# Performance work log

Measured on AMD Instinct MI355X. Metric: run time of the kernel, lower is better.

## Reference

```python
import jax, jax.numpy as jnp
import numpy as np

# Model dims
H = 1024          # hidden_size
I = 2048          # intermediate_size
E = 8             # num_experts
IE = I // E       # expert_intermediate_size = 256
V = 100000        # vocab_size
B, S = 8, 2048


def _rowwise_quantize(x):
    """Dynamic per-row int8 quantization (faithful to dynamic_quantize_int8, per_channel=True).
    Returns quantized values kept in float32 (identical values to int8->float cast) and per-row scale."""
    max_vals = jnp.max(jnp.abs(x), axis=-1, keepdims=True)
    scale = jnp.maximum(max_vals / 127.0, 1e-8)
    x_q = jnp.clip(jnp.round(x / scale), -128.0, 127.0)
    return x_q, scale[..., 0]


def _quantize_weight(w):
    """Per-output-channel int8 quantization of a [K, N] weight (as in from_float)."""
    max_vals = jnp.max(jnp.abs(w), axis=0, keepdims=True)      # [1, N]
    scale = jnp.maximum(max_vals / 127.0, 1e-8)
    w_q = jnp.clip(jnp.round(w / scale), -128.0, 127.0).astype(jnp.int8)
    return w_q, scale[0]


def setup_inputs() -> dict:
    key = jax.random.key(0)
    ks = jax.random.split(key, 6)
    hidden_states = jax.random.normal(ks[0], (B, S, H), dtype=jnp.float32)
    token_ids = jax.random.randint(ks[1], (B, S), 0, V, dtype=jnp.int32)

    # Pre-quantized expert weights (int8) with per-output-channel fp32 scales.
    gate_w = jax.random.normal(ks[2], (E, H, IE), dtype=jnp.float32) * 0.02
    up_w = jax.random.normal(ks[3], (E, H, IE), dtype=jnp.float32) * 0.02
    down_w = jax.random.normal(ks[4], (E, IE, H), dtype=jnp.float32) * 0.02
    gate_q, gate_scale = jax.vmap(_quantize_weight)(gate_w)   # [E,H,IE] int8, [E,IE]
    up_q, up_scale = jax.vmap(_quantize_weight)(up_w)         # [E,H,IE] int8, [E,IE]
    down_q, down_scale = jax.vmap(_quantize_weight)(down_w)   # [E,IE,H] int8, [E,H]

    # Deterministic contiguous token->expert mapping (V divisible by E here).
    token_to_expert = jnp.minimum(jnp.arange(V, dtype=jnp.int32) // (V // E), E - 1)

    return {
        "hidden_states": hidden_states,
        "token_ids": token_ids,
        "gate_q": gate_q, "gate_scale": gate_scale,
        "up_q": up_q, "up_scale": up_scale,
        "down_q": down_q, "down_scale": down_scale,
        "token_to_expert": token_to_expert,
    }


def reference(hidden_states, token_ids, gate_q, gate_scale, up_q, up_scale,
              down_q, down_scale, token_to_expert):
    Bh, Sh, Hh = hidden_states.shape
    n_exp = gate_q.shape[0]
    vocab = token_to_expert.shape[0]

    tid = jnp.clip(token_ids, 0, vocab - 1)
    expert_ids = token_to_expert[tid].reshape(-1)             # [T]

    x = hidden_states.reshape(-1, Hh)                          # [T, H]
    # Per-row activation quantization is expert-independent -> do it once for all tokens.
    x_q, x_s = _rowwise_quantize(x)                            # [T,H], [T]

    gq = gate_q.astype(jnp.float32)
    uq = up_q.astype(jnp.float32)
    dq = down_q.astype(jnp.float32)

    out = jnp.zeros_like(x)
    for e in range(n_exp):  # small fixed expert count
        # fused quantize-GEMM: int8 matmul + per-row activation scale + per-col weight scale
        gate = (x_q @ gq[e]) * x_s[:, None] * gate_scale[e][None, :]   # [T, IE]
        up = (x_q @ uq[e]) * x_s[:, None] * up_scale[e][None, :]       # [T, IE]
        inter = jax.nn.silu(gate) * up
        i_q, i_s = _rowwise_quantize(inter)
        o = (i_q @ dq[e]) * i_s[:, None] * down_scale[e][None, :]      # [T, H]
        out = jnp.where((expert_ids == e)[:, None], o, out)
    return out.reshape(Bh, Sh, Hh)
```

## Files before the change

kernel.cpp:

```cpp
#include <hip/hip_runtime.h>

typedef int   int4v   __attribute__((ext_vector_type(4)));
typedef float float4v __attribute__((ext_vector_type(4)));

#define T_TOK 16384
#define HD    1024
#define IE    256
#define EN    8
#define VSZ   100000

#define M_OFF 16
#define M_TS1 25

#define XQ_OFF   0ull
#define PB1_OFF  21053440ull
#define PB2_OFF  25247744ull
#define PERM_OFF 27344896ull
#define XS_OFF   27410688ull
#define META_OFF 27542272ull
#define BC_OFF   27542528ull
#define BB_OFF   27544576ull

__device__ __forceinline__ void gload16(const void* g, void* l) {
    __builtin_amdgcn_global_load_lds(
        (const __attribute__((address_space(1))) unsigned int*)g,
        (__attribute__((address_space(3))) unsigned int*)l,
        16, 0, 0);
}

__global__ void k_hist(const int* __restrict__ ids, const int* __restrict__ t2e,
                       int* __restrict__ bc) {
    __shared__ int h[EN];
    if (threadIdx.x < EN) h[threadIdx.x] = 0;
    __syncthreads();
    int t = blockIdx.x * 256 + threadIdx.x;
    int id = ids[t]; id = min(max(id, 0), VSZ - 1);
    atomicAdd(&h[t2e[id]], 1);
    __syncthreads();
    if (threadIdx.x < EN) bc[blockIdx.x * EN + threadIdx.x] = h[threadIdx.x];
}

__global__ __launch_bounds__(512) void k_scan(const int* __restrict__ bc,
                                              int* __restrict__ bbase,
                                              int* __restrict__ meta) {
    int e = threadIdx.x >> 6;
    int b = threadIdx.x & 63;
    int c = bc[b * EN + e];
    int inc = c;
    #pragma unroll
    for (int s = 1; s < 64; s <<= 1) {
        int v = __shfl_up(inc, s, 64);
        if (b >= s) inc += v;
    }
    int exc = inc - c;
    __shared__ int tot[EN];
    __shared__ int goff[EN];
    if (b == 63) tot[e] = inc;
    __syncthreads();
    if (threadIdx.x == 0) {
        int off = 0, t1 = 0;
        meta[M_OFF] = 0; meta[M_TS1] = 0;
        #pragma unroll
        for (int i = 0; i < EN; ++i) {
            goff[i] = off;
            int cc = tot[i];
            off += cc; t1 += (cc + 31) >> 5;
            meta[M_OFF + i + 1] = off;
            meta[M_TS1 + i + 1] = t1;
        }
    }
    __syncthreads();
    bbase[b * EN + e] = goff[e] + exc;
}

__global__ void k_assign(const int* __restrict__ ids, const int* __restrict__ t2e,
                         const int* __restrict__ bbase, int* __restrict__ perm) {
    __shared__ int cur[EN];
    if (threadIdx.x < EN) cur[threadIdx.x] = bbase[blockIdx.x * EN + threadIdx.x];
    __syncthreads();
    int t = blockIdx.x * 256 + threadIdx.x;
    int id = ids[t]; id = min(max(id, 0), VSZ - 1);
    int e = t2e[id];
    int slot = atomicAdd(&cur[e], 1);
    perm[slot] = t;
}

__global__ __launch_bounds__(256) void k_pre(const float* __restrict__ hidden,
                                             const int* __restrict__ gq,
                                             const int* __restrict__ uq,
                                             const int* __restrict__ dq,
                                             signed char* __restrict__ xq,
                                             float* __restrict__ xs,
                                             signed char* __restrict__ pb1,
                                             signed char* __restrict__ pb2) {
    int b = blockIdx.x;
    if (b < 4096) {
        int w = threadIdx.x >> 6, lane = threadIdx.x & 63;
        int token = (b << 2) + w;
        const float* row = hidden + (size_t)token * HD;
        float v[16];
        #pragma unroll
        for (int j = 0; j < 4; ++j) {
            float4v f = *(const float4v*)(row + lane * 16 + j * 4);
            v[j*4+0] = f[0]; v[j*4+1] = f[1]; v[j*4+2] = f[2]; v[j*4+3] = f[3];
        }
        float mx = 0.0f;
        #pragma unroll
        for (int j = 0; j < 16; ++j) mx = fmaxf(mx, fabsf(v[j]));
        #pragma unroll
        for (int s = 1; s < 64; s <<= 1) mx = fmaxf(mx, __shfl_xor(mx, s, 64));
        float sc = fmaxf(mx / 127.0f, 1e-8f);
        if (lane == 0) xs[token] = sc;
        int4v pk;
        #pragma unroll
        for (int j = 0; j < 4; ++j) {
            int bb[4];
            #pragma unroll
            for (int u = 0; u < 4; ++u) {
                float t = rintf(v[j*4+u] / sc);
                t = fminf(fmaxf(t, -128.0f), 127.0f);
                bb[u] = (int)t;
            }
            pk[j] = (bb[0] & 255) | ((bb[1] & 255) << 8) | ((bb[2] & 255) << 16) | (bb[3] << 24);
        }
        *(int4v*)(xq + (size_t)token * HD + lane * 16) = pk;
    } else {
        int idx = (b - 4096) * 256 + threadIdx.x;
        if (idx < 262144) {
            int n = idx & 511, kc = (idx >> 9) & 63, e = idx >> 15;
            const int* src = (n < 256) ? gq + (((size_t)((e << 10) + (kc << 4)) << 8) + n)
                                       : uq + (((size_t)((e << 10) + (kc << 4)) << 8) + (n - 256));
            int4v pk;
            #pragma unroll
            for (int jj = 0; jj < 4; ++jj) {
                int b0 = src[(size_t)(jj * 4 + 0) << 8], b1 = src[(size_t)(jj * 4 + 1) << 8];
                int b2 = src[(size_t)(jj * 4 + 2) << 8], b3 = src[(size_t)(jj * 4 + 3) << 8];
                pk[jj] = (b0 & 255) | ((b1 & 255) << 8) | ((b2 & 255) << 16) | (b3 << 24);
            }
            *(int4v*)(pb1 + ((size_t)((((e << 6) + kc) << 9) + n) << 4)) = pk;
        } else {
            int j = idx - 262144;
            int n = j & 1023, kc = (j >> 10) & 15, e = j >> 14;
            const int* src = dq + (((size_t)((e << 8) + (kc << 4)) << 10) + n);
            int4v pk;
            #pragma unroll
            for (int jj = 0; jj < 4; ++jj) {
                int b0 = src[(size_t)(jj * 4 + 0) << 10], b1 = src[(size_t)(jj * 4 + 1) << 10];
                int b2 = src[(size_t)(jj * 4 + 2) << 10], b3 = src[(size_t)(jj * 4 + 3) << 10];
                pk[jj] = (b0 & 255) | ((b1 & 255) << 8) | ((b2 & 255) << 16) | (b3 << 24);
            }
            *(int4v*)(pb2 + ((size_t)((((e << 4) + kc) << 10) + n) << 4)) = pk;
        }
    }
}

__global__ __launch_bounds__(256, 2) void k_mlp(const signed char* __restrict__ xq,
                                                const signed char* __restrict__ pb1,
                                                const signed char* __restrict__ pb2,
                                                const float* __restrict__ xs,
                                                const float* __restrict__ gsc,
                                                const float* __restrict__ usc,
                                                const float* __restrict__ dsc,
                                                const int* __restrict__ meta,
                                                const int* __restrict__ perm,
                                                float* __restrict__ out) {
    int b = (blockIdx.x & 7) * 65 + (blockIdx.x >> 3);
    int e = -1, m0 = 0, gend = 0;
    #pragma unroll
    for (int i = 0; i < EN; ++i) {
        int s0 = meta[M_TS1 + i], s1 = meta[M_TS1 + i + 1];
        if (b >= s0 && b < s1) { e = i; m0 = meta[M_OFF + i] + ((b - s0) << 5); gend = meta[M_OFF + i + 1]; }
    }
    if (e < 0) return;
    const int w = threadIdx.x >> 6, lane = threadIdx.x & 63;
    const int q = lane >> 4, r = lane & 15;

    __shared__ __align__(16) signed char lB[2][32768];
    __shared__ __align__(16) signed char arena[8192];
    float* pmax = (float*)(arena + 4096);
    float* rsc  = (float*)(arena + 4608);
    int*   ptok = (int*)(arena + 4736);

    if (threadIdx.x < 32) ptok[threadIdx.x] = perm[min(m0 + (int)threadIdx.x, T_TOK - 1)];
    __syncthreads();

    int tokr[2][4];
    #pragma unroll
    for (int mi = 0; mi < 2; ++mi)
        #pragma unroll
        for (int g = 0; g < 4; ++g)
            tokr[mi][g] = ptok[(mi << 4) + (q << 2) + g];

    const signed char* pbe1 = pb1 + (size_t)e * (64 * 512 * 16);
    const signed char* pbe2 = pb2 + (size_t)e * (16 * 1024 * 16);
    const int arow = (w << 4) + (lane >> 2);
    const int acq  = (lane & 3) ^ ((lane >> 2) & 3);
    const signed char* ga_base = xq + (size_t)ptok[arow & 31] * HD + (acq << 4);

    #define G1_STAGE(buf, kt)                                                          \
        {                                                                              \
            int kc0 = (kt) << 2;                                                       \
            _Pragma("unroll")                                                          \
            for (int j = 0; j < 8; ++j) {                                              \
                int n = ((j << 6) + lane) ^ ((w & 1) << 3);                            \
                gload16(pbe1 + (((size_t)(kc0 + w) * 512 + n) << 4),                   \
                        &lB[buf][((w << 3) + j) << 10]);                               \
            }                                                                          \
            if (w < 2) gload16(ga_base + ((kt) << 6), arena + ((buf) << 11) + (w << 10)); \
        }

    #define G2_STAGE(buf, st)                                                          \
        {                                                                              \
            int kc0 = ((st) & 3) << 2; int nhs = (st) >> 2;                            \
            _Pragma("unroll")                                                          \
            for (int j = 0; j < 8; ++j) {                                              \
                int n = ((j << 6) + lane) ^ ((w & 1) << 3);                            \
                gload16(pbe2 + (((size_t)(kc0 + w) * 1024 + (nhs << 9) + n) << 4),     \
                        &lB[buf][((w << 3) + j) << 10]);                               \
            }                                                                          \
        }

    int4v zero = {0, 0, 0, 0};
    int4v accg[2][4], accu[2][4];
    #pragma unroll
    for (int mi = 0; mi < 2; ++mi)
        #pragma unroll
        for (int i = 0; i < 4; ++i) { accg[mi][i] = zero; accu[mi][i] = zero; }

    G1_STAGE(0, 0);
    for (int kt = 0; kt < 16; ++kt) {
        int cur = kt & 1;
        __syncthreads();
        if (kt < 15) G1_STAGE(cur ^ 1, kt + 1);
        int4v a[2];
        #pragma unroll
        for (int mi = 0; mi < 2; ++mi)
            a[mi] = *(const int4v*)&arena[(cur << 11) + ((((mi << 4) + r) << 6) + ((q ^ (r & 3)) << 4))];
        #pragma unroll
        for (int i = 0; i < 4; ++i) {
            int n = (w << 6) + (i << 4) + r;
            int sg = (q << 9) + (n ^ ((q & 1) << 3));
            int su = (q << 9) + ((n + 256) ^ ((q & 1) << 3));
            int4v bg = *(const int4v*)&lB[cur][sg << 4];
            int4v bu = *(const int4v*)&lB[cur][su << 4];
            #pragma unroll
            for (int mi = 0; mi < 2; ++mi) {
                accg[mi][i] = __builtin_amdgcn_mfma_i32_16x16x64_i8(a[mi], bg, accg[mi][i], 0, 0, 0);
                accu[mi][i] = __builtin_amdgcn_mfma_i32_16x16x64_i8(a[mi], bu, accu[mi][i], 0, 0, 0);
            }
        }
    }
    #undef G1_STAGE

    G2_STAGE(0, 0);

    float gs[4], us[4];
    #pragma unroll
    for (int i = 0; i < 4; ++i) {
        int n = (w << 6) + (i << 4) + r;
        gs[i] = gsc[e * IE + n];
        us[i] = usc[e * IE + n];
    }
    float xsr[2][4];
    #pragma unroll
    for (int mi = 0; mi < 2; ++mi)
        #pragma unroll
        for (int g = 0; g < 4; ++g)
            xsr[mi][g] = xs[tokr[mi][g]];

    float inter[2][4][4];
    float pm[2][4];
    #pragma unroll
    for (int mi = 0; mi < 2; ++mi)
        #pragma unroll
        for (int g = 0; g < 4; ++g) {
            float mx = 0.0f;
            #pragma unroll
            for (int i = 0; i < 4; ++i) {
                float gv = (float)accg[mi][i][g] * xsr[mi][g] * gs[i];
                float uv = (float)accu[mi][i][g] * xsr[mi][g] * us[i];
                float sg = gv / (1.0f + expf(-gv));
                float vv = sg * uv;
                inter[mi][i][g] = vv;
                mx = fmaxf(mx, fabsf(vv));
            }
            #pragma unroll
            for (int s = 1; s < 16; s <<= 1) mx = fmaxf(mx, __shfl_xor(mx, s, 64));
            pm[mi][g] = mx;
        }

    __syncthreads();
    if (r == 0) {
        #pragma unroll
        for (int mi = 0; mi < 2; ++mi)
            #pragma unroll
            for (int g = 0; g < 4; ++g)
                pmax[(w << 5) + (mi << 4) + (q << 2) + g] = pm[mi][g];
    }
    __syncthreads();
    if (threadIdx.x < 32) {
        int row = threadIdx.x;
        float mx = fmaxf(fmaxf(pmax[row], pmax[32 + row]), fmaxf(pmax[64 + row], pmax[96 + row]));
        rsc[row] = fmaxf(mx / 127.0f, 1e-8f);
    }
    __syncthreads();
    float rscr[2][4];
    #pragma unroll
    for (int mi = 0; mi < 2; ++mi)
        #pragma unroll
        for (int g = 0; g < 4; ++g)
            rscr[mi][g] = rsc[(mi << 4) + (q << 2) + g];
    __syncthreads();

    #pragma unroll
    for (int mi = 0; mi < 2; ++mi)
        #pragma unroll
        for (int g = 0; g < 4; ++g) {
            int row = (mi << 4) + (q << 2) + g;
            float sc = rscr[mi][g];
            #pragma unroll
            for (int i = 0; i < 4; ++i) {
                float t = rintf(inter[mi][i][g] / sc);
                t = fminf(fmaxf(t, -128.0f), 127.0f);
                arena[(row << 8) + ((((w << 2) + i) ^ (row & 3)) << 4) + r] = (signed char)(int)t;
            }
        }

    int4v acc2[2][8];
    for (int st = 0; st < 8; ++st) {
        int cur = st & 1;
        __syncthreads();
        if (st < 7) G2_STAGE(cur ^ 1, st + 1);
        if ((st & 3) == 0) {
            #pragma unroll
            for (int mi = 0; mi < 2; ++mi)
                #pragma unroll
                for (int i = 0; i < 8; ++i) acc2[mi][i] = zero;
        }
        int4v a2[2];
        #pragma unroll
        for (int mi = 0; mi < 2; ++mi) {
            int row2 = (mi << 4) + r;
            a2[mi] = *(const int4v*)&arena[(row2 << 8) + (((((st & 3) << 2) + q) ^ (r & 3)) << 4)];
        }
        #pragma unroll
        for (int i = 0; i < 8; ++i) {
            int n = (w << 7) + (i << 4) + r;
            int sb = (q << 9) + (n ^ ((q & 1) << 3));
            int4v bb = *(const int4v*)&lB[cur][sb << 4];
            #pragma unroll
            for (int mi = 0; mi < 2; ++mi)
                acc2[mi][i] = __builtin_amdgcn_mfma_i32_16x16x64_i8(a2[mi], bb, acc2[mi][i], 0, 0, 0);
        }
        if ((st & 3) == 3) {
            int nhs = st >> 2;
            float ds[8];
            #pragma unroll
            for (int i = 0; i < 8; ++i)
                ds[i] = dsc[e * HD + (nhs << 9) + (w << 7) + (i << 4) + r];
            #pragma unroll
            for (int mi = 0; mi < 2; ++mi)
                #pragma unroll
                for (int g = 0; g < 4; ++g) {
                    int slot = m0 + (mi << 4) + (q << 2) + g;
                    if (slot < gend) {
                        size_t ob = (size_t)tokr[mi][g] * HD + (nhs << 9) + (w << 7) + r;
                        #pragma unroll
                        for (int i = 0; i < 8; ++i)
                            out[ob + (i << 4)] = (float)acc2[mi][i][g] * rscr[mi][g] * ds[i];
                    }
                }
        }
    }
    #undef G2_STAGE
}

extern "C" void kernel_launch(void* const* d_in, const int* in_sizes, int n_in,
                              void* d_out, int out_size, void* d_ws, size_t ws_size,
                              hipStream_t stream) {
    const float* hidden = (const float*)d_in[0];
    const int*   ids    = (const int*)d_in[1];
    const int*   gq     = (const int*)d_in[2];
    const float* gsc    = (const float*)d_in[3];
    const int*   uq     = (const int*)d_in[4];
    const float* usc    = (const float*)d_in[5];
    const int*   dq     = (const int*)d_in[6];
    const float* dsc    = (const float*)d_in[7];
    const int*   t2e    = (const int*)d_in[8];
    float* out = (float*)d_out;

    char* ws = (char*)d_ws;
    signed char* xq  = (signed char*)(ws + XQ_OFF);
    signed char* pb1 = (signed char*)(ws + PB1_OFF);
    signed char* pb2 = (signed char*)(ws + PB2_OFF);
    int*   perm = (int*)(ws + PERM_OFF);
    float* xs   = (float*)(ws + XS_OFF);
    int*   meta = (int*)(ws + META_OFF);
    int*   bc   = (int*)(ws + BC_OFF);
    int*   bbase= (int*)(ws + BB_OFF);

    k_hist<<<64, 256, 0, stream>>>(ids, t2e, bc);
    k_scan<<<1, 512, 0, stream>>>(bc, bbase, meta);
    k_assign<<<64, 256, 0, stream>>>(ids, t2e, bbase, perm);
    k_pre<<<5632, 256, 0, stream>>>(hidden, gq, uq, dq, xq, xs, pb1, pb2);
    k_mlp<<<520, 256, 0, stream>>>(xq, pb1, pb2, xs, gsc, usc, dsc, meta, perm, out);
}
```

Before: 204.6 us.

## Halve LDS staging buffers and load activations to registers for four-block occupancy

The per-stage weight buffers shrink from 32KB to 16KB each, and the gate and up tiles are now staged in alternate half-steps, doubling the pipeline step count. Activations are loaded straight from global memory into registers instead of through LDS, which also removes the token-index shared table and one barrier. Launch bounds rise from 2 to 4 blocks per CU to raise occupancy and hide latency. The cost is twice as many barriers per K loop and tighter register pressure, plus full unrolling of the loops.

```diff
diff --git a/kernel.cpp b/kernel.cpp
--- a/kernel.cpp
+++ b/kernel.cpp
@@ -154,7 +154,7 @@
     }
 }
 
-__global__ __launch_bounds__(256, 2) void k_mlp(const signed char* __restrict__ xq,
+__global__ __launch_bounds__(256, 4) void k_mlp(const signed char* __restrict__ xq,
                                                 const signed char* __restrict__ pb1,
                                                 const signed char* __restrict__ pb2,
                                                 const float* __restrict__ xs,
@@ -175,49 +175,44 @@
     const int w = threadIdx.x >> 6, lane = threadIdx.x & 63;
     const int q = lane >> 4, r = lane & 15;
 
-    __shared__ __align__(16) signed char lB[2][32768];
-    __shared__ __align__(16) signed char arena[8192];
-    float* pmax = (float*)(arena + 4096);
-    float* rsc  = (float*)(arena + 4608);
-    int*   ptok = (int*)(arena + 4736);
-
-    if (threadIdx.x < 32) ptok[threadIdx.x] = perm[min(m0 + (int)threadIdx.x, T_TOK - 1)];
-    __syncthreads();
-
-    int tokr[2][4];
-    #pragma unroll
-    for (int mi = 0; mi < 2; ++mi)
-        #pragma unroll
-        for (int g = 0; g < 4; ++g)
-            tokr[mi][g] = ptok[(mi << 4) + (q << 2) + g];
+    __shared__ __align__(16) signed char lB[2][16384];
+    __shared__ __align__(16) signed char iqt[8192];
+    float* pmax = (float*)iqt;
+    float* rscp = (float*)(iqt + 512);
+
+    int tokA0 = perm[min(m0 + r, T_TOK - 1)];
+    int tokA1 = perm[min(m0 + 16 + r, T_TOK - 1)];
+    const signed char* aptr0 = xq + (size_t)tokA0 * HD + (q << 4);
+    const signed char* aptr1 = xq + (size_t)tokA1 * HD + (q << 4);
 
     const signed char* pbe1 = pb1 + (size_t)e * (64 * 512 * 16);
     const signed char* pbe2 = pb2 + (size_t)e * (16 * 1024 * 16);
-    const int arow = (w << 4) + (lane >> 2);
-    const int acq  = (lane & 3) ^ ((lane >> 2) & 3);
-    const signed char* ga_base = xq + (size_t)ptok[arow & 31] * HD + (acq << 4);
-
-    #define G1_STAGE(buf, kt)                                                          \
-        {                                                                              \
-            int kc0 = (kt) << 2;                                                       \
-            _Pragma("unroll")                                                          \
-            for (int j = 0; j < 8; ++j) {                                              \
-                int n = ((j << 6) + lane) ^ ((w & 1) << 3);                            \
-                gload16(pbe1 + (((size_t)(kc0 + w) * 512 + n) << 4),                   \
-                        &lB[buf][((w << 3) + j) << 10]);                               \
-            }                                                                          \
-            if (w < 2) gload16(ga_base + ((kt) << 6), arena + ((buf) << 11) + (w << 10)); \
-        }
-
-    #define G2_STAGE(buf, st)                                                          \
-        {                                                                              \
-            int kc0 = ((st) & 3) << 2; int nhs = (st) >> 2;                            \
-            _Pragma("unroll")                                                          \
-            for (int j = 0; j < 8; ++j) {                                              \
-                int n = ((j << 6) + lane) ^ ((w & 1) << 3);                            \
-                gload16(pbe2 + (((size_t)(kc0 + w) * 1024 + (nhs << 9) + n) << 4),     \
-                        &lB[buf][((w << 3) + j) << 10]);                               \
-            }                                                                          \
+
+    #define G1S(buf, g, h)                                                         \
+        {                                                                          \
+            const signed char* srow = pbe1 +                                       \
+                (((size_t)((((g) << 2) + w) * 512 + ((h) << 8))) << 4);            \
+            _Pragma("unroll")                                                      \
+            for (int j = 0; j < 4; ++j) {                                          \
+                int nx = ((j << 6) + lane) ^ ((w & 1) << 3);                       \
+                gload16(srow + ((size_t)nx << 4), &lB[buf][((w << 2) + j) << 10]); \
+            }                                                                      \
+        }
+    #define G1A(g)                                                                 \
+        {                                                                          \
+            areg[(g) & 1][0] = *(const int4v*)(aptr0 + ((g) << 6));                \
+            areg[(g) & 1][1] = *(const int4v*)(aptr1 + ((g) << 6));                \
+        }
+    #define G2S(buf, st2)                                                          \
+        {                                                                          \
+            int nh2 = (st2) >> 3, g22 = ((st2) >> 1) & 3, ch2 = (st2) & 1;         \
+            const signed char* srow = pbe2 +                                       \
+                (((size_t)(((g22 << 2) + w) * 1024 + (nh2 << 9) + (ch2 << 8))) << 4); \
+            _Pragma("unroll")                                                      \
+            for (int j = 0; j < 4; ++j) {                                          \
+                int nx = ((j << 6) + lane) ^ ((w & 1) << 3);                       \
+                gload16(srow + ((size_t)nx << 4), &lB[buf][((w << 2) + j) << 10]); \
+            }                                                                      \
         }
 
     int4v zero = {0, 0, 0, 0};
@@ -227,33 +222,49 @@
         #pragma unroll
         for (int i = 0; i < 4; ++i) { accg[mi][i] = zero; accu[mi][i] = zero; }
 
-    G1_STAGE(0, 0);
-    for (int kt = 0; kt < 16; ++kt) {
-        int cur = kt & 1;
+    int4v areg[2][2];
+    G1S(0, 0, 0);
+    G1A(0);
+
+    #pragma unroll
+    for (int s = 0; s < 32; ++s) {
         __syncthreads();
-        if (kt < 15) G1_STAGE(cur ^ 1, kt + 1);
-        int4v a[2];
-        #pragma unroll
-        for (int mi = 0; mi < 2; ++mi)
-            a[mi] = *(const int4v*)&arena[(cur << 11) + ((((mi << 4) + r) << 6) + ((q ^ (r & 3)) << 4))];
+        const int nxt = s + 1;
+        if (nxt < 32) {
+            G1S(nxt & 1, nxt >> 1, nxt & 1);
+            if ((nxt & 1) == 0) G1A(nxt >> 1);
+        }
+        const int g = s >> 1, h = s & 1, cur = s & 1;
+        int4v a0 = areg[g & 1][0], a1 = areg[g & 1][1];
         #pragma unroll
         for (int i = 0; i < 4; ++i) {
-            int n = (w << 6) + (i << 4) + r;
-            int sg = (q << 9) + (n ^ ((q & 1) << 3));
-            int su = (q << 9) + ((n + 256) ^ ((q & 1) << 3));
-            int4v bg = *(const int4v*)&lB[cur][sg << 4];
-            int4v bu = *(const int4v*)&lB[cur][su << 4];
-            #pragma unroll
-            for (int mi = 0; mi < 2; ++mi) {
-                accg[mi][i] = __builtin_amdgcn_mfma_i32_16x16x64_i8(a[mi], bg, accg[mi][i], 0, 0, 0);
-                accu[mi][i] = __builtin_amdgcn_mfma_i32_16x16x64_i8(a[mi], bu, accu[mi][i], 0, 0, 0);
-            }
-        }
-    }
-    #undef G1_STAGE
-
-    G2_STAGE(0, 0);
-
+            int nl = (w << 6) + (i << 4) + r;
+            int sl = (q << 8) + (nl ^ ((q & 1) << 3));
+            int4v bb = *(const int4v*)&lB[cur][sl << 4];
+            if (h == 0) {
+                accg[0][i] = __builtin_amdgcn_mfma_i32_16x16x64_i8(a0, bb, accg[0][i], 0, 0, 0);
+                accg[1][i] = __builtin_amdgcn_mfma_i32_16x16x64_i8(a1, bb, accg[1][i], 0, 0, 0);
+            } else {
+                accu[0][i] = __builtin_amdgcn_mfma_i32_16x16x64_i8(a0, bb, accu[0][i], 0, 0, 0);
+                accu[1][i] = __builtin_amdgcn_mfma_i32_16x16x64_i8(a1, bb, accu[1][i], 0, 0, 0);
+            }
+        }
+    }
+    #undef G1S
+    #undef G1A
+
+    G2S(0, 0);
+
+    int tokr[2][4];
+    float xsr[2][4];
+    #pragma unroll
+    for (int mi = 0; mi < 2; ++mi)
+        #pragma unroll
+        for (int g2 = 0; g2 < 4; ++g2) {
+            int slot = m0 + (mi << 4) + (q << 2) + g2;
+            tokr[mi][g2] = perm[min(slot, T_TOK - 1)];
+            xsr[mi][g2] = xs[tokr[mi][g2]];
+        }
     float gs[4], us[4];
     #pragma unroll
     for (int i = 0; i < 4; ++i) {
@@ -261,118 +272,120 @@
         gs[i] = gsc[e * IE + n];
         us[i] = usc[e * IE + n];
     }
-    float xsr[2][4];
-    #pragma unroll
-    for (int mi = 0; mi < 2; ++mi)
-        #pragma unroll
-        for (int g = 0; g < 4; ++g)
-            xsr[mi][g] = xs[tokr[mi][g]];
+    float ds[2][2][4];
+    #pragma unroll
+    for (int nh = 0; nh < 2; ++nh)
+        #pragma unroll
+        for (int ch = 0; ch < 2; ++ch)
+            #pragma unroll
+            for (int i = 0; i < 4; ++i)
+                ds[nh][ch][i] = dsc[e * HD + (nh << 9) + (ch << 8) + (w << 6) + (i << 4) + r];
 
     float inter[2][4][4];
     float pm[2][4];
     #pragma unroll
     for (int mi = 0; mi < 2; ++mi)
         #pragma unroll
-        for (int g = 0; g < 4; ++g) {
+        for (int g2 = 0; g2 < 4; ++g2) {
             float mx = 0.0f;
             #pragma unroll
             for (int i = 0; i < 4; ++i) {
-                float gv = (float)accg[mi][i][g] * xsr[mi][g] * gs[i];
-                float uv = (float)accu[mi][i][g] * xsr[mi][g] * us[i];
+                float gv = (float)accg[mi][i][g2] * xsr[mi][g2] * gs[i];
+                float uv = (float)accu[mi][i][g2] * xsr[mi][g2] * us[i];
                 float sg = gv / (1.0f + expf(-gv));
                 float vv = sg * uv;
-                inter[mi][i][g] = vv;
+                inter[mi][i][g2] = vv;
                 mx = fmaxf(mx, fabsf(vv));
             }
             #pragma unroll
             for (int s = 1; s < 16; s <<= 1) mx = fmaxf(mx, __shfl_xor(mx, s, 64));
-            pm[mi][g] = mx;
-        }
-
-    __syncthreads();
+            pm[mi][g2] = mx;
+        }
+
     if (r == 0) {
         #pragma unroll
         for (int mi = 0; mi < 2; ++mi)
             #pragma unroll
-            for (int g = 0; g < 4; ++g)
-                pmax[(w << 5) + (mi << 4) + (q << 2) + g] = pm[mi][g];
+            for (int g2 = 0; g2 < 4; ++g2)
+                pmax[(w << 5) + (mi << 4) + (q << 2) + g2] = pm[mi][g2];
     }
     __syncthreads();
     if (threadIdx.x < 32) {
         int row = threadIdx.x;
         float mx = fmaxf(fmaxf(pmax[row], pmax[32 + row]), fmaxf(pmax[64 + row], pmax[96 + row]));
-        rsc[row] = fmaxf(mx / 127.0f, 1e-8f);
+        rscp[row] = fmaxf(mx / 127.0f, 1e-8f);
     }
     __syncthreads();
     float rscr[2][4];
     #pragma unroll
     for (int mi = 0; mi < 2; ++mi)
         #pragma unroll
-        for (int g = 0; g < 4; ++g)
-            rscr[mi][g] = rsc[(mi << 4) + (q << 2) + g];
+        for (int g2 = 0; g2 < 4; ++g2)
+            rscr[mi][g2] = rscp[(mi << 4) + (q << 2) + g2];
     __syncthreads();
 
     #pragma unroll
     for (int mi = 0; mi < 2; ++mi)
         #pragma unroll
-        for (int g = 0; g < 4; ++g) {
-            int row = (mi << 4) + (q << 2) + g;
-            float sc = rscr[mi][g];
+        for (int g2 = 0; g2 < 4; ++g2) {
+            int row = (mi << 4) + (q << 2) + g2;
+            float sc = rscr[mi][g2];
             #pragma unroll
             for (int i = 0; i < 4; ++i) {
-                float t = rintf(inter[mi][i][g] / sc);
+                float t = rintf(inter[mi][i][g2] / sc);
                 t = fminf(fmaxf(t, -128.0f), 127.0f);
-                arena[(row << 8) + ((((w << 2) + i) ^ (row & 3)) << 4) + r] = (signed char)(int)t;
-            }
-        }
-
-    int4v acc2[2][8];
-    for (int st = 0; st < 8; ++st) {
-        int cur = st & 1;
+                iqt[(row << 8) + ((((w << 2) + i) ^ (row & 3)) << 4) + r] = (signed char)(int)t;
+            }
+        }
+
+    int4v acc2[2][2][4];
+    #pragma unroll
+    for (int st = 0; st < 16; ++st) {
         __syncthreads();
-        if (st < 7) G2_STAGE(cur ^ 1, st + 1);
-        if ((st & 3) == 0) {
+        const int nxt2 = st + 1;
+        if (nxt2 < 16) { G2S(nxt2 & 1, nxt2); }
+        if ((st & 7) == 0) {
             #pragma unroll
             for (int mi = 0; mi < 2; ++mi)
                 #pragma unroll
-                for (int i = 0; i < 8; ++i) acc2[mi][i] = zero;
-        }
+                for (int ch = 0; ch < 2; ++ch)
+                    #pragma unroll
+                    for (int i = 0; i < 4; ++i) acc2[mi][ch][i] = zero;
+        }
+        const int nh = st >> 3, g2v = (st >> 1) & 3, ch = st & 1, cur = st & 1;
         int4v a2[2];
         #pragma unroll
         for (int mi = 0; mi < 2; ++mi) {
             int row2 = (mi << 4) + r;
-            a2[mi] = *(const int4v*)&arena[(row2 << 8) + (((((st & 3) << 2) + q) ^ (r & 3)) << 4)];
-        }
-        #pragma unroll
-        for (int i = 0; i < 8; ++i) {
-            int n = (w << 7) + (i << 4) + r;
-            int sb = (q << 9) + (n ^ ((q & 1) << 3));
-            int4v bb = *(const int4v*)&lB[cur][sb << 4];
-            #pragma unroll
-            for (int mi = 0; mi < 2; ++mi)
-                acc2[mi][i] = __builtin_amdgcn_mfma_i32_16x16x64_i8(a2[mi], bb, acc2[mi][i], 0, 0, 0);
-        }
-        if ((st & 3) == 3) {
-            int nhs = st >> 2;
-            float ds[8];
-            #pragma unroll
-            for (int i = 0; i < 8; ++i)
-                ds[i] = dsc[e * HD + (nhs << 9) + (w << 7) + (i << 4) + r];
+            a2[mi] = *(const int4v*)&iqt[(row2 << 8) + ((((g2v << 2) + q) ^ (r & 3)) << 4)];
+        }
+        #pragma unroll
+        for (int i = 0; i < 4; ++i) {
+            int nl = (w << 6) + (i << 4) + r;
+            int sl = (q << 8) + (nl ^ ((q & 1) << 3));
+            int4v bb = *(const int4v*)&lB[cur][sl << 4];
+            acc2[0][ch][i] = __builtin_amdgcn_mfma_i32_16x16x64_i8(a2[0], bb, acc2[0][ch][i], 0, 0, 0);
+            acc2[1][ch][i] = __builtin_amdgcn_mfma_i32_16x16x64_i8(a2[1], bb, acc2[1][ch][i], 0, 0, 0);
+        }
+        if ((st & 7) == 7) {
             #pragma unroll
             for (int mi = 0; mi < 2; ++mi)
                 #pragma unroll
-                for (int g = 0; g < 4; ++g) {
-                    int slot = m0 + (mi << 4) + (q << 2) + g;
+                for (int g2 = 0; g2 < 4; ++g2) {
+                    int slot = m0 + (mi << 4) + (q << 2) + g2;
                     if (slot < gend) {
-                        size_t ob = (size_t)tokr[mi][g] * HD + (nhs << 9) + (w << 7) + r;
+                        size_t ob = (size_t)tokr[mi][g2] * HD + (nh << 9) + (w << 6) + r;
                         #pragma unroll
-                        for (int i = 0; i < 8; ++i)
-                            out[ob + (i << 4)] = (float)acc2[mi][i][g] * rscr[mi][g] * ds[i];
+                        for (int ch2 = 0; ch2 < 2; ++ch2)
+                            #pragma unroll
+                            for (int i = 0; i < 4; ++i)
+                                out[ob + (ch2 << 8) + (i << 4)] =
+                                    (float)acc2[mi][ch2][i][g2] * rscr[mi][g2] * ds[nh][ch2][i];
                     }
                 }
         }
     }
-    #undef G2_STAGE
+    #undef G2S
 }
 
 extern "C" void kernel_launch(void* const* d_in, const int* in_sizes, int n_in,
```

Measured after the change: 225.5 us. 1.1x slower.
